# Performance work log

Measured on AMD Instinct MI355X. Metric: run time of the kernel, lower is better.

## Reference

```python
import jax, jax.numpy as jnp
import numpy as np

N, D, B, E, K, H, C = 100000, 256, 20000, 16, 3, 256, 40  # m = K = 3


def setup_inputs() -> dict:
    key = jax.random.key(0)
    ks = jax.random.split(key, 11)
    return {
        "nodes": jax.random.randint(ks[0], (B,), 0, N, dtype=jnp.int32),
        "structure": jax.random.randint(ks[1], (B, E, K), 0, N, dtype=jnp.int32),
        "X": jax.random.normal(ks[2], (N, D), dtype=jnp.float32),
        "beta": jax.random.uniform(ks[3], (1,), dtype=jnp.float32),
        "w_att_w": jax.random.normal(ks[4], (1,), dtype=jnp.float32),
        "w_att_b": jax.random.normal(ks[5], (1,), dtype=jnp.float32),
        "lin_W": jax.random.normal(ks[6], (H, D), dtype=jnp.float32) * 0.05,
        "lin_b": jax.random.normal(ks[7], (H,), dtype=jnp.float32) * 0.05,
        "skip_W": jax.random.normal(ks[8], (H, D), dtype=jnp.float32) * 0.05,
        "cls_W": jax.random.normal(ks[9], (C, H), dtype=jnp.float32) * 0.05,
        "cls_b": jax.random.normal(ks[10], (C,), dtype=jnp.float32) * 0.05,
    }


def reference(nodes, structure, X, beta, w_att_w, w_att_b, lin_W, lin_b, skip_W, cls_W, cls_b):
    # --- TMessagePassing (batched over nodes and hyperedges) ---
    feats = X[structure]                                  # [B, E, K, D] gather
    # variance over nodes in the hyperedge (unbiased=False), mean over feature dim
    edge_var = jnp.var(feats, axis=2).mean(axis=-1)       # [B, E]
    att = jax.nn.sigmoid(w_att_w[0] * edge_var + w_att_b[0])  # [B, E]
    # len(edge) == m (K == m=3): msg = prod(feats[:-1], dim=0)
    msg = jnp.prod(feats[:, :, : K - 1, :], axis=2)       # [B, E, D]
    neigh = jnp.einsum("be,bed->bd", att, msg)            # sum of att * msg over edges
    # --- Encoder (combine == 'sum') ---
    self_feat = X[nodes]                                  # [B, D]
    h = self_feat + neigh
    enc = jax.nn.relu(h @ lin_W.T + lin_b)                # [B, H]
    enc = (1.0 - beta[0]) * enc + beta[0] * (self_feat @ skip_W.T)
    # --- classifier + log_softmax ---
    logits = enc @ cls_W.T + cls_b                        # [B, C]
    return jax.nn.log_softmax(logits, axis=1)
```

## Files before the change

kernel.cpp:

```cpp
#include <hip/hip_runtime.h>
#include <hip/hip_bf16.h>
#include <math.h>

#define Dn 256
#define En 16
#define Kn 3
#define Hn 256
#define Cn 40
#define CnP 48

typedef __attribute__((ext_vector_type(8)))  short bf16x8;
typedef __attribute__((ext_vector_type(4)))  float f32x4;
typedef __attribute__((ext_vector_type(16))) float f32x16;

static __device__ __forceinline__ float bf2f(unsigned short u) {
    return __uint_as_float(((unsigned)u) << 16);
}
static __device__ __forceinline__ unsigned short f2bfbits(float v) {
    __hip_bfloat16 hb = __float2bfloat16(v);
    return *reinterpret_cast<unsigned short*>(&hb);
}
static __device__ __forceinline__ unsigned pack2bf(float a, float b) {
    return (unsigned)f2bfbits(a) | ((unsigned)f2bfbits(b) << 16);
}
static __device__ __forceinline__ unsigned swz(unsigned boff) {
    return boff ^ (((boff >> 9) & 7u) << 4);
}

__global__ __launch_bounds__(256) void conv_all(
    const float* __restrict__ X, const float* __restrict__ linW,
    const float* __restrict__ skipW, const float* __restrict__ clsW,
    uint4* __restrict__ Xb, uint4* __restrict__ linWb,
    uint4* __restrict__ skipWb, uint4* __restrict__ clsWb,
    int x8, int w8)
{
    int t = blockIdx.x * 256 + threadIdx.x;
    const int c8 = (CnP * Hn) / 8;
    if (t < x8) {
        const float4* iv = reinterpret_cast<const float4*>(X);
        const float4 a = iv[(size_t)t * 2 + 0];
        const float4 b = iv[(size_t)t * 2 + 1];
        Xb[t] = (uint4){pack2bf(a.x, a.y), pack2bf(a.z, a.w),
                        pack2bf(b.x, b.y), pack2bf(b.z, b.w)};
        return;
    }
    t -= x8;
    if (t < w8) {
        const float4* iv = reinterpret_cast<const float4*>(linW);
        const float4 a = iv[(size_t)t * 2 + 0];
        const float4 b = iv[(size_t)t * 2 + 1];
        linWb[t] = (uint4){pack2bf(a.x, a.y), pack2bf(a.z, a.w),
                           pack2bf(b.x, b.y), pack2bf(b.z, b.w)};
        return;
    }
    t -= w8;
    if (t < w8) {
        const float4* iv = reinterpret_cast<const float4*>(skipW);
        const float4 a = iv[(size_t)t * 2 + 0];
        const float4 b = iv[(size_t)t * 2 + 1];
        skipWb[t] = (uint4){pack2bf(a.x, a.y), pack2bf(a.z, a.w),
                            pack2bf(b.x, b.y), pack2bf(b.z, b.w)};
        return;
    }
    t -= w8;
    if (t < c8) {
        const int row = t >> 5;
        if (row < Cn) {
            const float4* iv = reinterpret_cast<const float4*>(clsW);
            const float4 a = iv[(size_t)t * 2 + 0];
            const float4 b = iv[(size_t)t * 2 + 1];
            clsWb[t] = (uint4){pack2bf(a.x, a.y), pack2bf(a.z, a.w),
                               pack2bf(b.x, b.y), pack2bf(b.z, b.w)};
        } else {
            clsWb[t] = (uint4){0u, 0u, 0u, 0u};
        }
    }
}

__global__ __launch_bounds__(256) void mp_kernel_bf(
    const int* __restrict__ nodes, const int* __restrict__ structure,
    const uint2* __restrict__ Xb,
    const float* __restrict__ waw_p, const float* __restrict__ wab_p,
    uint2* __restrict__ h_out, uint2* __restrict__ self_out, int B)
{
    const int wave = threadIdx.x >> 6;
    const int lane = threadIdx.x & 63;
    const int b = blockIdx.x * 4 + wave;
    if (b >= B) return;
    const int ub = __builtin_amdgcn_readfirstlane(b);

    const float waw = waw_p[0];
    const float wab = wab_p[0];

    float4 neigh = make_float4(0.f, 0.f, 0.f, 0.f);
    const int* st = structure + (size_t)ub * (En * Kn);

    #pragma unroll 1
    for (int g = 0; g < En / 4; ++g) {
        int idx[12];
        #pragma unroll
        for (int u = 0; u < 12; ++u) idx[u] = st[g * 12 + u];

        uint2 r0[4], r1[4], r2[4];
        #pragma unroll
        for (int u = 0; u < 4; ++u) {
            r0[u] = Xb[(size_t)idx[u * 3 + 0] * (Dn / 4) + lane];
            r1[u] = Xb[(size_t)idx[u * 3 + 1] * (Dn / 4) + lane];
            r2[u] = Xb[(size_t)idx[u * 3 + 2] * (Dn / 4) + lane];
        }

        float pv[4];
        float4 msg[4];
        #pragma unroll
        for (int u = 0; u < 4; ++u) {
            float4 f0, f1, f2;
            f0.x = bf2f((unsigned short)(r0[u].x & 0xffff));
            f0.y = bf2f((unsigned short)(r0[u].x >> 16));
            f0.z = bf2f((unsigned short)(r0[u].y & 0xffff));
            f0.w = bf2f((unsigned short)(r0[u].y >> 16));
            f1.x = bf2f((unsigned short)(r1[u].x & 0xffff));
            f1.y = bf2f((unsigned short)(r1[u].x >> 16));
            f1.z = bf2f((unsigned short)(r1[u].y & 0xffff));
            f1.w = bf2f((unsigned short)(r1[u].y >> 16));
            f2.x = bf2f((unsigned short)(r2[u].x & 0xffff));
            f2.y = bf2f((unsigned short)(r2[u].x >> 16));
            f2.z = bf2f((unsigned short)(r2[u].y & 0xffff));
            f2.w = bf2f((unsigned short)(r2[u].y >> 16));

            float s2 = 0.f, cr = 0.f, tt;
            s2 = fmaf(f0.x, f0.x, s2); s2 = fmaf(f1.x, f1.x, s2); s2 = fmaf(f2.x, f2.x, s2);
            tt = f1.x + f2.x; cr = fmaf(f0.x, tt, cr); cr = fmaf(f1.x, f2.x, cr);
            s2 = fmaf(f0.y, f0.y, s2); s2 = fmaf(f1.y, f1.y, s2); s2 = fmaf(f2.y, f2.y, s2);
            tt = f1.y + f2.y; cr = fmaf(f0.y, tt, cr); cr = fmaf(f1.y, f2.y, cr);
            s2 = fmaf(f0.z, f0.z, s2); s2 = fmaf(f1.z, f1.z, s2); s2 = fmaf(f2.z, f2.z, s2);
            tt = f1.z + f2.z; cr = fmaf(f0.z, tt, cr); cr = fmaf(f1.z, f2.z, cr);
            s2 = fmaf(f0.w, f0.w, s2); s2 = fmaf(f1.w, f1.w, s2); s2 = fmaf(f2.w, f2.w, s2);
            tt = f1.w + f2.w; cr = fmaf(f0.w, tt, cr); cr = fmaf(f1.w, f2.w, cr);

            pv[u] = s2 - cr;
            msg[u].x = f0.x * f1.x;
            msg[u].y = f0.y * f1.y;
            msg[u].z = f0.z * f1.z;
            msg[u].w = f0.w * f1.w;
        }

        #pragma unroll
        for (int off = 32; off; off >>= 1) {
            #pragma unroll
            for (int u = 0; u < 4; ++u) pv[u] += __shfl_xor(pv[u], off);
        }

        #pragma unroll
        for (int u = 0; u < 4; ++u) {
            const float var_mean = pv[u] * (2.f / (9.f * (float)Dn));
            const float att = 1.f / (1.f + expf(-(waw * var_mean + wab)));
            neigh.x += att * msg[u].x;
            neigh.y += att * msg[u].y;
            neigh.z += att * msg[u].z;
            neigh.w += att * msg[u].w;
        }
    }

    const uint2 sv = Xb[(size_t)nodes[ub] * (Dn / 4) + lane];
    self_out[(size_t)b * (Dn / 4) + lane] = sv;
    const float sx = bf2f((unsigned short)(sv.x & 0xffff));
    const float sy = bf2f((unsigned short)(sv.x >> 16));
    const float sz = bf2f((unsigned short)(sv.y & 0xffff));
    const float sw = bf2f((unsigned short)(sv.y >> 16));
    uint2 o;
    o.x = pack2bf(sx + neigh.x, sy + neigh.y);
    o.y = pack2bf(sz + neigh.z, sw + neigh.w);
    h_out[(size_t)b * (Dn / 4) + lane] = o;
}

__global__ __launch_bounds__(256, 2) void enc_cls_fused(
    const unsigned short* __restrict__ hB,
    const unsigned short* __restrict__ selfB,
    const unsigned short* __restrict__ linWb, const float* __restrict__ linb,
    const unsigned short* __restrict__ skipWb, const float* __restrict__ beta_p,
    const unsigned short* __restrict__ clsWb,
    const float* __restrict__ clsb,
    float* __restrict__ out, int M)
{
    __shared__ unsigned short elds[32 * 256];

    const int w  = threadIdx.x >> 6;
    const int l  = threadIdx.x & 63;
    const int lr = l & 31;
    const int kh = l >> 5;
    const int row0 = blockIdx.x * 32;

    const int arow = row0 + lr;
    const int arc  = arow < M ? arow : (M - 1);
    const int bc0 = w * 64 + lr;
    const int bc1 = w * 64 + 32 + lr;

    f32x16 acc1[2], acc2[2];
    acc1[0] = (f32x16)(0.f); acc1[1] = (f32x16)(0.f);
    acc2[0] = (f32x16)(0.f); acc2[1] = (f32x16)(0.f);

    #pragma unroll 4
    for (int k0 = 0; k0 < Dn; k0 += 16) {
        const int ko = k0 + kh * 8;
        const bf16x8 a1  = *reinterpret_cast<const bf16x8*>(hB    + (size_t)arc * Dn + ko);
        const bf16x8 a2  = *reinterpret_cast<const bf16x8*>(selfB + (size_t)arc * Dn + ko);
        const bf16x8 b10 = *reinterpret_cast<const bf16x8*>(linWb  + (size_t)bc0 * Dn + ko);
        const bf16x8 b11 = *reinterpret_cast<const bf16x8*>(linWb  + (size_t)bc1 * Dn + ko);
        const bf16x8 b20 = *reinterpret_cast<const bf16x8*>(skipWb + (size_t)bc0 * Dn + ko);
        const bf16x8 b21 = *reinterpret_cast<const bf16x8*>(skipWb + (size_t)bc1 * Dn + ko);
        acc1[0] = __builtin_amdgcn_mfma_f32_32x32x16_bf16(a1, b10, acc1[0], 0, 0, 0);
        acc1[1] = __builtin_amdgcn_mfma_f32_32x32x16_bf16(a1, b11, acc1[1], 0, 0, 0);
        acc2[0] = __builtin_amdgcn_mfma_f32_32x32x16_bf16(a2, b20, acc2[0], 0, 0, 0);
        acc2[1] = __builtin_amdgcn_mfma_f32_32x32x16_bf16(a2, b21, acc2[1], 0, 0, 0);
    }

    const float beta = beta_p[0];
    const float omb = 1.f - beta;
    #pragma unroll
    for (int n = 0; n < 2; ++n) {
        const int col = w * 64 + n * 32 + lr;
        const float bias = linb[col];
        #pragma unroll
        for (int r = 0; r < 16; ++r) {
            const int rowl = (r & 3) + 8 * (r >> 2) + 4 * kh;
            const float c1 = fmaxf(acc1[n][r] + bias, 0.f);
            const unsigned short v = f2bfbits(omb * c1 + beta * acc2[n][r]);
            const unsigned boff = swz((unsigned)(rowl * 512 + col * 2));
            *reinterpret_cast<unsigned short*>(
                reinterpret_cast<char*>(elds) + boff) = v;
        }
    }
    __syncthreads();

    if (w < 2) {
        const int lr16 = l & 15;
        const int kg = l >> 4;
        const int rowl0 = w * 16 + lr16;

        f32x4 cacc[3];
        cacc[0] = (f32x4){0.f,0.f,0.f,0.f};
        cacc[1] = (f32x4){0.f,0.f,0.f,0.f};
        cacc[2] = (f32x4){0.f,0.f,0.f,0.f};

        #pragma unroll
        for (int k0 = 0; k0 < Hn; k0 += 32) {
            const int ko = k0 + kg * 8;
            const unsigned boff = swz((unsigned)(rowl0 * 512 + ko * 2));
            const bf16x8 a = *reinterpret_cast<const bf16x8*>(
                reinterpret_cast<const char*>(elds) + boff);
            #pragma unroll
            for (int t = 0; t < 3; ++t) {
                const bf16x8 bb = *reinterpret_cast<const bf16x8*>(
                    clsWb + (size_t)(t * 16 + lr16) * Hn + ko);
                cacc[t] = __builtin_amdgcn_mfma_f32_16x16x32_bf16(a, bb, cacc[t], 0, 0, 0);
            }
        }

        float bias3[3];
        #pragma unroll
        for (int t = 0; t < 3; ++t) {
            const int cb = t * 16 + lr16;
            bias3[t] = (cb < Cn) ? clsb[cb] : -INFINITY;
        }

        #pragma unroll
        for (int r = 0; r < 4; ++r) {
            float lg0 = cacc[0][r] + bias3[0];
            float lg1 = cacc[1][r] + bias3[1];
            float lg2 = cacc[2][r] + bias3[2];
            float mx = fmaxf(fmaxf(lg0, lg1), lg2);
            #pragma unroll
            for (int off = 8; off; off >>= 1) mx = fmaxf(mx, __shfl_xor(mx, off));
            float se = expf(lg0 - mx) + expf(lg1 - mx) + expf(lg2 - mx);
            #pragma unroll
            for (int off = 8; off; off >>= 1) se += __shfl_xor(se, off);
            const float lse = logf(se);

            const int row = row0 + w * 16 + kg * 4 + r;
            if (row < M) {
                if (lr16 < 8) out[(size_t)row * Cn + 32 + lr16] = lg2 - mx - lse;
                out[(size_t)row * Cn + lr16]      = lg0 - mx - lse;
                out[(size_t)row * Cn + 16 + lr16] = lg1 - mx - lse;
            }
        }
    }
}

__global__ __launch_bounds__(256) void mp_kernel_f32(
    const int* __restrict__ nodes, const int* __restrict__ structure,
    const float* __restrict__ X, const float* __restrict__ waw_p,
    const float* __restrict__ wab_p, float* __restrict__ h_out, int B)
{
    const int wave = threadIdx.x >> 6;
    const int lane = threadIdx.x & 63;
    const int b = blockIdx.x * 4 + wave;
    if (b >= B) return;
    const int ub = __builtin_amdgcn_readfirstlane(b);

    const float waw = waw_p[0];
    const float wab = wab_p[0];
    const float4* __restrict__ Xv = reinterpret_cast<const float4*>(X);

    float4 neigh = make_float4(0.f, 0.f, 0.f, 0.f);
    const int* st = structure + (size_t)ub * (En * Kn);

    #pragma unroll 1
    for (int e = 0; e < En; ++e) {
        const int i0 = st[e * 3 + 0];
        const int i1 = st[e * 3 + 1];
        const int i2 = st[e * 3 + 2];
        const float4 f0 = Xv[(size_t)i0 * (Dn / 4) + lane];
        const float4 f1 = Xv[(size_t)i1 * (Dn / 4) + lane];
        const float4 f2 = Xv[(size_t)i2 * (Dn / 4) + lane];
        float pv = 0.f;
        {
            float a, bb, c, m;
            a = f0.x; bb = f1.x; c = f2.x;
            m = (a + bb + c) * (1.f / 3.f);
            pv += (a * a + bb * bb + c * c) * (1.f / 3.f) - m * m;
            a = f0.y; bb = f1.y; c = f2.y;
            m = (a + bb + c) * (1.f / 3.f);
            pv += (a * a + bb * bb + c * c) * (1.f / 3.f) - m * m;
            a = f0.z; bb = f1.z; c = f2.z;
            m = (a + bb + c) * (1.f / 3.f);
            pv += (a * a + bb * bb + c * c) * (1.f / 3.f) - m * m;
            a = f0.w; bb = f1.w; c = f2.w;
            m = (a + bb + c) * (1.f / 3.f);
            pv += (a * a + bb * bb + c * c) * (1.f / 3.f) - m * m;
        }
        #pragma unroll
        for (int off = 32; off; off >>= 1) pv += __shfl_xor(pv, off);
        const float var_mean = pv * (1.f / (float)Dn);
        const float att = 1.f / (1.f + expf(-(waw * var_mean + wab)));
        neigh.x += att * f0.x * f1.x;
        neigh.y += att * f0.y * f1.y;
        neigh.z += att * f0.z * f1.z;
        neigh.w += att * f0.w * f1.w;
    }

    const float4 s = Xv[(size_t)nodes[ub] * (Dn / 4) + lane];
    float4 h;
    h.x = s.x + neigh.x; h.y = s.y + neigh.y;
    h.z = s.z + neigh.z; h.w = s.w + neigh.w;
    reinterpret_cast<float4*>(h_out)[(size_t)b * (Dn / 4) + lane] = h;
}

#define BM 64
#define BN 64
#define BKs 16
#define LDT 68

__global__ __launch_bounds__(256) void enc_gemm_f32(
    const float* __restrict__ hA, const int* __restrict__ nodes,
    const float* __restrict__ X,
    const float* __restrict__ linW, const float* __restrict__ linb,
    const float* __restrict__ skipW, const float* __restrict__ beta_p,
    float* __restrict__ enc2, int M)
{
    __shared__ float Ats1[BKs][LDT];
    __shared__ float Ats2[BKs][LDT];
    __shared__ float Bts1[BKs][LDT];
    __shared__ float Bts2[BKs][LDT];

    const int tid = threadIdx.x;
    const int tx = tid & 15;
    const int ty = tid >> 4;
    const int row0 = blockIdx.x * BM;
    const int col0 = blockIdx.y * BN;

    const int lr = tid >> 2;
    const int lc = tid & 3;

    const int arow = row0 + lr;
    const bool arow_ok = arow < M;
    const int self_row = arow_ok ? nodes[arow] : 0;

    float acc1[4][4] = {{0.f}}, acc2[4][4] = {{0.f}};

    for (int k0 = 0; k0 < Dn; k0 += BKs) {
        float4 a1v = make_float4(0.f, 0.f, 0.f, 0.f);
        float4 a2v = make_float4(0.f, 0.f, 0.f, 0.f);
        if (arow_ok) {
            a1v = *reinterpret_cast<const float4*>(hA + (size_t)arow * Dn + k0 + lc * 4);
            a2v = *reinterpret_cast<const float4*>(X + (size_t)self_row * Dn + k0 + lc * 4);
        }
        const float4 b1v = *reinterpret_cast<const float4*>(linW + (size_t)(col0 + lr) * Dn + k0 + lc * 4);
        const float4 b2v = *reinterpret_cast<const float4*>(skipW + (size_t)(col0 + lr) * Dn + k0 + lc * 4);

        __syncthreads();
        Ats1[lc * 4 + 0][lr] = a1v.x; Ats1[lc * 4 + 1][lr] = a1v.y;
        Ats1[lc * 4 + 2][lr] = a1v.z; Ats1[lc * 4 + 3][lr] = a1v.w;
        Ats2[lc * 4 + 0][lr] = a2v.x; Ats2[lc * 4 + 1][lr] = a2v.y;
        Ats2[lc * 4 + 2][lr] = a2v.z; Ats2[lc * 4 + 3][lr] = a2v.w;
        Bts1[lc * 4 + 0][lr] = b1v.x; Bts1[lc * 4 + 1][lr] = b1v.y;
        Bts1[lc * 4 + 2][lr] = b1v.z; Bts1[lc * 4 + 3][lr] = b1v.w;
        Bts2[lc * 4 + 0][lr] = b2v.x; Bts2[lc * 4 + 1][lr] = b2v.y;
        Bts2[lc * 4 + 2][lr] = b2v.z; Bts2[lc * 4 + 3][lr] = b2v.w;
        __syncthreads();

        #pragma unroll
        for (int kk = 0; kk < BKs; ++kk) {
            const float4 a1 = *reinterpret_cast<const float4*>(&Ats1[kk][ty * 4]);
            const float4 a2 = *reinterpret_cast<const float4*>(&Ats2[kk][ty * 4]);
            const float4 b1 = *reinterpret_cast<const float4*>(&Bts1[kk][tx * 4]);
            const float4 b2 = *reinterpret_cast<const float4*>(&Bts2[kk][tx * 4]);
            const float a1a[4] = {a1.x, a1.y, a1.z, a1.w};
            const float a2a[4] = {a2.x, a2.y, a2.z, a2.w};
            const float b1a[4] = {b1.x, b1.y, b1.z, b1.w};
            const float b2a[4] = {b2.x, b2.y, b2.z, b2.w};
            #pragma unroll
            for (int i = 0; i < 4; ++i)
                #pragma unroll
                for (int j = 0; j < 4; ++j) {
                    acc1[i][j] = fmaf(a1a[i], b1a[j], acc1[i][j]);
                    acc2[i][j] = fmaf(a2a[i], b2a[j], acc2[i][j]);
                }
        }
    }

    const float beta = beta_p[0];
    const float omb = 1.f - beta;
    #pragma unroll
    for (int i = 0; i < 4; ++i) {
        const int r = row0 + ty * 4 + i;
        if (r >= M) continue;
        #pragma unroll
        for (int j = 0; j < 4; ++j) {
            const int c = col0 + tx * 4 + j;
            float c1 = acc1[i][j] + linb[c];
            c1 = fmaxf(c1, 0.f);
            enc2[(size_t)r * Hn + c] = omb * c1 + beta * acc2[i][j];
        }
    }
}

__global__ __launch_bounds__(256) void cls_kernel_f32(
    const float* __restrict__ enc2, const float* __restrict__ clsW,
    const float* __restrict__ clsb, float* __restrict__ out, int B)
{
    const int wave = threadIdx.x >> 6;
    const int lane = threadIdx.x & 63;
    const int b = blockIdx.x * 4 + wave;
    if (b >= B) return;

    const float4 e = reinterpret_cast<const float4*>(enc2 + (size_t)b * Hn)[lane];
    const float4* __restrict__ clsWv = reinterpret_cast<const float4*>(clsW);

    float mylogit = -INFINITY;
    #pragma unroll
    for (int c0 = 0; c0 < Cn; c0 += 8) {
        float p[8];
        #pragma unroll
        for (int u = 0; u < 8; ++u) {
            const float4 wv = clsWv[(size_t)(c0 + u) * (Hn / 4) + lane];
            p[u] = e.x * wv.x + e.y * wv.y + e.z * wv.z + e.w * wv.w;
        }
        #pragma unroll
        for (int off = 32; off; off >>= 1) {
            #pragma unroll
            for (int u = 0; u < 8; ++u) p[u] += __shfl_xor(p[u], off);
        }
        #pragma unroll
        for (int u = 0; u < 8; ++u)
            if (lane == c0 + u) mylogit = p[u];
    }
    if (lane < Cn) mylogit += clsb[lane];

    float mx = mylogit;
    #pragma unroll
    for (int off = 32; off; off >>= 1) mx = fmaxf(mx, __shfl_xor(mx, off));
    float ex = (lane < Cn) ? expf(mylogit - mx) : 0.f;
    float se = ex;
    #pragma unroll
    for (int off = 32; off; off >>= 1) se += __shfl_xor(se, off);
    const float lse = logf(se);

    if (lane < Cn) out[(size_t)b * Cn + lane] = mylogit - mx - lse;
}

extern "C" void kernel_launch(void* const* d_in, const int* in_sizes, int n_in,
                              void* d_out, int out_size, void* d_ws, size_t ws_size,
                              hipStream_t stream) {
    const int*   nodes     = (const int*)d_in[0];
    const int*   structure = (const int*)d_in[1];
    const float* X         = (const float*)d_in[2];
    const float* beta      = (const float*)d_in[3];
    const float* waw       = (const float*)d_in[4];
    const float* wab       = (const float*)d_in[5];
    const float* linW      = (const float*)d_in[6];
    const float* linb      = (const float*)d_in[7];
    const float* skipW     = (const float*)d_in[8];
    const float* clsW      = (const float*)d_in[9];
    const float* clsb      = (const float*)d_in[10];
    float* out = (float*)d_out;

    const int B = in_sizes[0];
    const int Ntot = in_sizes[2];

    unsigned short* h_bf   = (unsigned short*)d_ws;
    unsigned short* selfb  = h_bf + (size_t)B * Dn;
    unsigned short* Xb     = selfb + (size_t)B * Dn;
    unsigned short* linWb  = Xb + (size_t)Ntot;
    unsigned short* skipWb = linWb + (size_t)Hn * Dn;
    unsigned short* clsWb  = skipWb + (size_t)Hn * Dn;

    const size_t need = ((size_t)B * Dn * 2 + (size_t)Ntot +
                         (size_t)Hn * Dn * 2 + (size_t)CnP * Hn) * 2;

    if (ws_size >= need) {
        const int x8 = Ntot / 8;
        const int w8 = (Hn * Dn) / 8;
        const int c8 = (CnP * Hn) / 8;
        const int G = x8 + 2 * w8 + c8;
        conv_all<<<(G + 255) / 256, 256, 0, stream>>>(
            X, linW, skipW, clsW,
            (uint4*)Xb, (uint4*)linWb, (uint4*)skipWb, (uint4*)clsWb, x8, w8);

        mp_kernel_bf<<<(B + 3) / 4, 256, 0, stream>>>(
            nodes, structure, (const uint2*)Xb, waw, wab,
            (uint2*)h_bf, (uint2*)selfb, B);

        enc_cls_fused<<<(B + 31) / 32, 256, 0, stream>>>(
            h_bf, selfb, linWb, linb, skipWb, beta, clsWb, clsb, out, B);
    } else {
        float* enc2 = (float*)d_ws;
        float* hf   = enc2 + (size_t)B * Hn;
        mp_kernel_f32<<<(B + 3) / 4, 256, 0, stream>>>(nodes, structure, X, waw, wab, hf, B);
        dim3 g2((B + BM - 1) / BM, Hn / BN);
        enc_gemm_f32<<<g2, 256, 0, stream>>>(hf, nodes, X, linW, linb, skipW, beta, enc2, B);
        cls_kernel_f32<<<(B + 3) / 4, 256, 0, stream>>>(enc2, clsW, clsb, out, B);
    }
}
```

Measured before the change: 138.4 us.

## Fuse message-passing gather into encoder/classifier GEMM kernel via LDS staging

Merges the per-node hypergraph message-passing kernel with the encoder+classifier MFMA kernel. Each 256-thread block gathers 32 rows (8 per wave), stores h and self features as bf16 into swizzled shared memory, then runs the two GEMMs and the log-softmax from LDS. The intermediate h/self global writes and reads and one launch go away. In exchange each block now does a serial gather phase before its MFMA phase, which limits overlap, and it uses more LDS, which may lower occupancy.

```diff
diff --git a/kernel.cpp b/kernel.cpp
--- a/kernel.cpp
+++ b/kernel.cpp
@@ -23,8 +23,8 @@
 static __device__ __forceinline__ unsigned pack2bf(float a, float b) {
     return (unsigned)f2bfbits(a) | ((unsigned)f2bfbits(b) << 16);
 }
-static __device__ __forceinline__ unsigned swz(unsigned boff) {
-    return boff ^ (((boff >> 9) & 7u) << 4);
+static __device__ __forceinline__ unsigned swz5(unsigned boff) {
+    return boff ^ (((boff >> 9) & 31u) << 4);
 }
 
 __global__ __launch_bounds__(256) void conv_all(
@@ -77,133 +77,134 @@
     }
 }
 
-__global__ __launch_bounds__(256) void mp_kernel_bf(
+__global__ __launch_bounds__(256, 4) void mp_enc_cls(
     const int* __restrict__ nodes, const int* __restrict__ structure,
     const uint2* __restrict__ Xb,
     const float* __restrict__ waw_p, const float* __restrict__ wab_p,
-    uint2* __restrict__ h_out, uint2* __restrict__ self_out, int B)
+    const unsigned short* __restrict__ linWb, const float* __restrict__ linb,
+    const unsigned short* __restrict__ skipWb, const float* __restrict__ beta_p,
+    const unsigned short* __restrict__ clsWb, const float* __restrict__ clsb,
+    float* __restrict__ out, int B)
 {
-    const int wave = threadIdx.x >> 6;
+    __shared__ unsigned short hlds[32 * 256];
+    __shared__ unsigned short slds[32 * 256];
+
+    const int wid  = threadIdx.x >> 6;
     const int lane = threadIdx.x & 63;
-    const int b = blockIdx.x * 4 + wave;
-    if (b >= B) return;
-    const int ub = __builtin_amdgcn_readfirstlane(b);
+    const int row0 = blockIdx.x * 32;
 
     const float waw = waw_p[0];
     const float wab = wab_p[0];
 
-    float4 neigh = make_float4(0.f, 0.f, 0.f, 0.f);
-    const int* st = structure + (size_t)ub * (En * Kn);
-
     #pragma unroll 1
-    for (int g = 0; g < En / 4; ++g) {
-        int idx[12];
-        #pragma unroll
-        for (int u = 0; u < 12; ++u) idx[u] = st[g * 12 + u];
-
-        uint2 r0[4], r1[4], r2[4];
-        #pragma unroll
-        for (int u = 0; u < 4; ++u) {
-            r0[u] = Xb[(size_t)idx[u * 3 + 0] * (Dn / 4) + lane];
-            r1[u] = Xb[(size_t)idx[u * 3 + 1] * (Dn / 4) + lane];
-            r2[u] = Xb[(size_t)idx[u * 3 + 2] * (Dn / 4) + lane];
-        }
-
-        float pv[4];
-        float4 msg[4];
-        #pragma unroll
-        for (int u = 0; u < 4; ++u) {
-            float4 f0, f1, f2;
-            f0.x = bf2f((unsigned short)(r0[u].x & 0xffff));
-            f0.y = bf2f((unsigned short)(r0[u].x >> 16));
-            f0.z = bf2f((unsigned short)(r0[u].y & 0xffff));
-            f0.w = bf2f((unsigned short)(r0[u].y >> 16));
-            f1.x = bf2f((unsigned short)(r1[u].x & 0xffff));
-            f1.y = bf2f((unsigned short)(r1[u].x >> 16));
-            f1.z = bf2f((unsigned short)(r1[u].y & 0xffff));
-            f1.w = bf2f((unsigned short)(r1[u].y >> 16));
-            f2.x = bf2f((unsigned short)(r2[u].x & 0xffff));
-            f2.y = bf2f((unsigned short)(r2[u].x >> 16));
-            f2.z = bf2f((unsigned short)(r2[u].y & 0xffff));
-            f2.w = bf2f((unsigned short)(r2[u].y >> 16));
-
-            float s2 = 0.f, cr = 0.f, tt;
-            s2 = fmaf(f0.x, f0.x, s2); s2 = fmaf(f1.x, f1.x, s2); s2 = fmaf(f2.x, f2.x, s2);
-            tt = f1.x + f2.x; cr = fmaf(f0.x, tt, cr); cr = fmaf(f1.x, f2.x, cr);
-            s2 = fmaf(f0.y, f0.y, s2); s2 = fmaf(f1.y, f1.y, s2); s2 = fmaf(f2.y, f2.y, s2);
-            tt = f1.y + f2.y; cr = fmaf(f0.y, tt, cr); cr = fmaf(f1.y, f2.y, cr);
-            s2 = fmaf(f0.z, f0.z, s2); s2 = fmaf(f1.z, f1.z, s2); s2 = fmaf(f2.z, f2.z, s2);
-            tt = f1.z + f2.z; cr = fmaf(f0.z, tt, cr); cr = fmaf(f1.z, f2.z, cr);
-            s2 = fmaf(f0.w, f0.w, s2); s2 = fmaf(f1.w, f1.w, s2); s2 = fmaf(f2.w, f2.w, s2);
-            tt = f1.w + f2.w; cr = fmaf(f0.w, tt, cr); cr = fmaf(f1.w, f2.w, cr);
-
-            pv[u] = s2 - cr;
-            msg[u].x = f0.x * f1.x;
-            msg[u].y = f0.y * f1.y;
-            msg[u].z = f0.z * f1.z;
-            msg[u].w = f0.w * f1.w;
-        }
-
-        #pragma unroll
-        for (int off = 32; off; off >>= 1) {
-            #pragma unroll
-            for (int u = 0; u < 4; ++u) pv[u] += __shfl_xor(pv[u], off);
-        }
-
-        #pragma unroll
-        for (int u = 0; u < 4; ++u) {
-            const float var_mean = pv[u] * (2.f / (9.f * (float)Dn));
-            const float att = 1.f / (1.f + expf(-(waw * var_mean + wab)));
-            neigh.x += att * msg[u].x;
-            neigh.y += att * msg[u].y;
-            neigh.z += att * msg[u].z;
-            neigh.w += att * msg[u].w;
-        }
-    }
-
-    const uint2 sv = Xb[(size_t)nodes[ub] * (Dn / 4) + lane];
-    self_out[(size_t)b * (Dn / 4) + lane] = sv;
-    const float sx = bf2f((unsigned short)(sv.x & 0xffff));
-    const float sy = bf2f((unsigned short)(sv.x >> 16));
-    const float sz = bf2f((unsigned short)(sv.y & 0xffff));
-    const float sw = bf2f((unsigned short)(sv.y >> 16));
-    uint2 o;
-    o.x = pack2bf(sx + neigh.x, sy + neigh.y);
-    o.y = pack2bf(sz + neigh.z, sw + neigh.w);
-    h_out[(size_t)b * (Dn / 4) + lane] = o;
-}
-
-__global__ __launch_bounds__(256, 2) void enc_cls_fused(
-    const unsigned short* __restrict__ hB,
-    const unsigned short* __restrict__ selfB,
-    const unsigned short* __restrict__ linWb, const float* __restrict__ linb,
-    const unsigned short* __restrict__ skipWb, const float* __restrict__ beta_p,
-    const unsigned short* __restrict__ clsWb,
-    const float* __restrict__ clsb,
-    float* __restrict__ out, int M)
-{
-    __shared__ unsigned short elds[32 * 256];
-
-    const int w  = threadIdx.x >> 6;
-    const int l  = threadIdx.x & 63;
-    const int lr = l & 31;
-    const int kh = l >> 5;
-    const int row0 = blockIdx.x * 32;
-
-    const int arow = row0 + lr;
-    const int arc  = arow < M ? arow : (M - 1);
-    const int bc0 = w * 64 + lr;
-    const int bc1 = w * 64 + 32 + lr;
+    for (int j = 0; j < 8; ++j) {
+        const int rowl = wid * 8 + j;
+        const int b = row0 + rowl;
+        if (b < B) {
+            const int ub = __builtin_amdgcn_readfirstlane(b);
+            const int* st = structure + (size_t)ub * (En * Kn);
+
+            float4 neigh = make_float4(0.f, 0.f, 0.f, 0.f);
+
+            #pragma unroll 1
+            for (int g = 0; g < En / 4; ++g) {
+                int idx[12];
+                #pragma unroll
+                for (int u = 0; u < 12; ++u) idx[u] = st[g * 12 + u];
+
+                uint2 r0[4], r1[4], r2[4];
+                #pragma unroll
+                for (int u = 0; u < 4; ++u) {
+                    r0[u] = Xb[(size_t)idx[u * 3 + 0] * (Dn / 4) + lane];
+                    r1[u] = Xb[(size_t)idx[u * 3 + 1] * (Dn / 4) + lane];
+                    r2[u] = Xb[(size_t)idx[u * 3 + 2] * (Dn / 4) + lane];
+                }
+
+                float pv[4];
+                float4 msg[4];
+                #pragma unroll
+                for (int u = 0; u < 4; ++u) {
+                    float4 f0, f1, f2;
+                    f0.x = bf2f((unsigned short)(r0[u].x & 0xffff));
+                    f0.y = bf2f((unsigned short)(r0[u].x >> 16));
+                    f0.z = bf2f((unsigned short)(r0[u].y & 0xffff));
+                    f0.w = bf2f((unsigned short)(r0[u].y >> 16));
+                    f1.x = bf2f((unsigned short)(r1[u].x & 0xffff));
+                    f1.y = bf2f((unsigned short)(r1[u].x >> 16));
+                    f1.z = bf2f((unsigned short)(r1[u].y & 0xffff));
+                    f1.w = bf2f((unsigned short)(r1[u].y >> 16));
+                    f2.x = bf2f((unsigned short)(r2[u].x & 0xffff));
+                    f2.y = bf2f((unsigned short)(r2[u].x >> 16));
+                    f2.z = bf2f((unsigned short)(r2[u].y & 0xffff));
+                    f2.w = bf2f((unsigned short)(r2[u].y >> 16));
+
+                    float s2 = 0.f, cr = 0.f, tt;
+                    s2 = fmaf(f0.x, f0.x, s2); s2 = fmaf(f1.x, f1.x, s2); s2 = fmaf(f2.x, f2.x, s2);
+                    tt = f1.x + f2.x; cr = fmaf(f0.x, tt, cr); cr = fmaf(f1.x, f2.x, cr);
+                    s2 = fmaf(f0.y, f0.y, s2); s2 = fmaf(f1.y, f1.y, s2); s2 = fmaf(f2.y, f2.y, s2);
+                    tt = f1.y + f2.y; cr = fmaf(f0.y, tt, cr); cr = fmaf(f1.y, f2.y, cr);
+                    s2 = fmaf(f0.z, f0.z, s2); s2 = fmaf(f1.z, f1.z, s2); s2 = fmaf(f2.z, f2.z, s2);
+                    tt = f1.z + f2.z; cr = fmaf(f0.z, tt, cr); cr = fmaf(f1.z, f2.z, cr);
+                    s2 = fmaf(f0.w, f0.w, s2); s2 = fmaf(f1.w, f1.w, s2); s2 = fmaf(f2.w, f2.w, s2);
+                    tt = f1.w + f2.w; cr = fmaf(f0.w, tt, cr); cr = fmaf(f1.w, f2.w, cr);
+
+                    pv[u] = s2 - cr;
+                    msg[u].x = f0.x * f1.x;
+                    msg[u].y = f0.y * f1.y;
+                    msg[u].z = f0.z * f1.z;
+                    msg[u].w = f0.w * f1.w;
+                }
+
+                #pragma unroll
+                for (int off = 32; off; off >>= 1) {
+                    #pragma unroll
+                    for (int u = 0; u < 4; ++u) pv[u] += __shfl_xor(pv[u], off);
+                }
+
+                #pragma unroll
+                for (int u = 0; u < 4; ++u) {
+                    const float var_mean = pv[u] * (2.f / (9.f * (float)Dn));
+                    const float att = 1.f / (1.f + expf(-(waw * var_mean + wab)));
+                    neigh.x += att * msg[u].x;
+                    neigh.y += att * msg[u].y;
+                    neigh.z += att * msg[u].z;
+                    neigh.w += att * msg[u].w;
+                }
+            }
+
+            const uint2 sv = Xb[(size_t)nodes[ub] * (Dn / 4) + lane];
+            const float sx = bf2f((unsigned short)(sv.x & 0xffff));
+            const float sy = bf2f((unsigned short)(sv.x >> 16));
+            const float sz = bf2f((unsigned short)(sv.y & 0xffff));
+            const float sw = bf2f((unsigned short)(sv.y >> 16));
+            uint2 o;
+            o.x = pack2bf(sx + neigh.x, sy + neigh.y);
+            o.y = pack2bf(sz + neigh.z, sw + neigh.w);
+
+            const unsigned boff = swz5((unsigned)(rowl * 512 + lane * 8));
+            *reinterpret_cast<uint2*>(reinterpret_cast<char*>(slds) + boff) = sv;
+            *reinterpret_cast<uint2*>(reinterpret_cast<char*>(hlds) + boff) = o;
+        }
+    }
+    __syncthreads();
+
+    const int lr = lane & 31;
+    const int kh = lane >> 5;
+    const int bc0 = wid * 64 + lr;
+    const int bc1 = wid * 64 + 32 + lr;
 
     f32x16 acc1[2], acc2[2];
     acc1[0] = (f32x16)(0.f); acc1[1] = (f32x16)(0.f);
     acc2[0] = (f32x16)(0.f); acc2[1] = (f32x16)(0.f);
 
-    #pragma unroll 4
+    #pragma unroll 2
     for (int k0 = 0; k0 < Dn; k0 += 16) {
         const int ko = k0 + kh * 8;
-        const bf16x8 a1  = *reinterpret_cast<const bf16x8*>(hB    + (size_t)arc * Dn + ko);
-        const bf16x8 a2  = *reinterpret_cast<const bf16x8*>(selfB + (size_t)arc * Dn + ko);
+        const unsigned aoff = swz5((unsigned)(lr * 512 + ko * 2));
+        const bf16x8 a1 = *reinterpret_cast<const bf16x8*>(
+            reinterpret_cast<const char*>(hlds) + aoff);
+        const bf16x8 a2 = *reinterpret_cast<const bf16x8*>(
+            reinterpret_cast<const char*>(slds) + aoff);
         const bf16x8 b10 = *reinterpret_cast<const bf16x8*>(linWb  + (size_t)bc0 * Dn + ko);
         const bf16x8 b11 = *reinterpret_cast<const bf16x8*>(linWb  + (size_t)bc1 * Dn + ko);
         const bf16x8 b20 = *reinterpret_cast<const bf16x8*>(skipWb + (size_t)bc0 * Dn + ko);
@@ -213,29 +214,30 @@
         acc2[0] = __builtin_amdgcn_mfma_f32_32x32x16_bf16(a2, b20, acc2[0], 0, 0, 0);
         acc2[1] = __builtin_amdgcn_mfma_f32_32x32x16_bf16(a2, b21, acc2[1], 0, 0, 0);
     }
+    __syncthreads();
 
     const float beta = beta_p[0];
     const float omb = 1.f - beta;
     #pragma unroll
     for (int n = 0; n < 2; ++n) {
-        const int col = w * 64 + n * 32 + lr;
+        const int col = wid * 64 + n * 32 + lr;
         const float bias = linb[col];
         #pragma unroll
         for (int r = 0; r < 16; ++r) {
             const int rowl = (r & 3) + 8 * (r >> 2) + 4 * kh;
             const float c1 = fmaxf(acc1[n][r] + bias, 0.f);
             const unsigned short v = f2bfbits(omb * c1 + beta * acc2[n][r]);
-            const unsigned boff = swz((unsigned)(rowl * 512 + col * 2));
+            const unsigned boff = swz5((unsigned)(rowl * 512 + col * 2));
             *reinterpret_cast<unsigned short*>(
-                reinterpret_cast<char*>(elds) + boff) = v;
+                reinterpret_cast<char*>(hlds) + boff) = v;
         }
     }
     __syncthreads();
 
-    if (w < 2) {
-        const int lr16 = l & 15;
-        const int kg = l >> 4;
-        const int rowl0 = w * 16 + lr16;
+    if (wid < 2) {
+        const int lr16 = lane & 15;
+        const int kg = lane >> 4;
+        const int rowl0 = wid * 16 + lr16;
 
         f32x4 cacc[3];
         cacc[0] = (f32x4){0.f,0.f,0.f,0.f};
@@ -245,9 +247,9 @@
         #pragma unroll
         for (int k0 = 0; k0 < Hn; k0 += 32) {
             const int ko = k0 + kg * 8;
-            const unsigned boff = swz((unsigned)(rowl0 * 512 + ko * 2));
+            const unsigned boff = swz5((unsigned)(rowl0 * 512 + ko * 2));
             const bf16x8 a = *reinterpret_cast<const bf16x8*>(
-                reinterpret_cast<const char*>(elds) + boff);
+                reinterpret_cast<const char*>(hlds) + boff);
             #pragma unroll
             for (int t = 0; t < 3; ++t) {
                 const bf16x8 bb = *reinterpret_cast<const bf16x8*>(
@@ -276,8 +278,8 @@
             for (int off = 8; off; off >>= 1) se += __shfl_xor(se, off);
             const float lse = logf(se);
 
-            const int row = row0 + w * 16 + kg * 4 + r;
-            if (row < M) {
+            const int row = row0 + wid * 16 + kg * 4 + r;
+            if (row < B) {
                 if (lr16 < 8) out[(size_t)row * Cn + 32 + lr16] = lg2 - mx - lse;
                 out[(size_t)row * Cn + lr16]      = lg0 - mx - lse;
                 out[(size_t)row * Cn + 16 + lr16] = lg1 - mx - lse;
@@ -497,15 +499,12 @@
     const int B = in_sizes[0];
     const int Ntot = in_sizes[2];
 
-    unsigned short* h_bf   = (unsigned short*)d_ws;
-    unsigned short* selfb  = h_bf + (size_t)B * Dn;
-    unsigned short* Xb     = selfb + (size_t)B * Dn;
+    unsigned short* Xb     = (unsigned short*)d_ws;
     unsigned short* linWb  = Xb + (size_t)Ntot;
     unsigned short* skipWb = linWb + (size_t)Hn * Dn;
     unsigned short* clsWb  = skipWb + (size_t)Hn * Dn;
 
-    const size_t need = ((size_t)B * Dn * 2 + (size_t)Ntot +
-                         (size_t)Hn * Dn * 2 + (size_t)CnP * Hn) * 2;
+    const size_t need = ((size_t)Ntot + (size_t)Hn * Dn * 2 + (size_t)CnP * Hn) * 2;
 
     if (ws_size >= need) {
         const int x8 = Ntot / 8;
@@ -516,12 +515,9 @@
             X, linW, skipW, clsW,
             (uint4*)Xb, (uint4*)linWb, (uint4*)skipWb, (uint4*)clsWb, x8, w8);
 
-        mp_kernel_bf<<<(B + 3) / 4, 256, 0, stream>>>(
+        mp_enc_cls<<<(B + 31) / 32, 256, 0, stream>>>(
             nodes, structure, (const uint2*)Xb, waw, wab,
-            (uint2*)h_bf, (uint2*)selfb, B);
-
-        enc_cls_fused<<<(B + 31) / 32, 256, 0, stream>>>(
-            h_bf, selfb, linWb, linb, skipWb, beta, clsWb, clsb, out, B);
+            linWb, linb, skipWb, beta, clsWb, clsb, out, B);
     } else {
         float* enc2 = (float*)d_ws;
         float* hf   = enc2 + (size_t)B * Hn;
```

Result: faster. 124.2 us (-10.3%).

## Shrink encoder row tile to 16 using 16x16x32 MFMA for higher occupancy

Applied to the files above, without the earlier changes.

The fused encoder+classifier kernel now processes 16 rows per block instead of 32, switching from 32x32x16 to 16x16x32 bf16 MFMA with four 16-column tiles per wave. This halves the shared staging buffer and the accumulator registers, and raises the launch-bounds occupancy hint from 2 to 8 blocks. The cost is twice as many blocks, each re-reading the full lin/skip weight matrices, so global and L2 traffic for weights doubles. The classifier stage now runs on a single wave per block.

```diff
diff --git a/kernel.cpp b/kernel.cpp
--- a/kernel.cpp
+++ b/kernel.cpp
@@ -11,7 +11,6 @@
 
 typedef __attribute__((ext_vector_type(8)))  short bf16x8;
 typedef __attribute__((ext_vector_type(4)))  float f32x4;
-typedef __attribute__((ext_vector_type(16))) float f32x16;
 
 static __device__ __forceinline__ float bf2f(unsigned short u) {
     return __uint_as_float(((unsigned)u) << 16);
@@ -23,8 +22,8 @@
 static __device__ __forceinline__ unsigned pack2bf(float a, float b) {
     return (unsigned)f2bfbits(a) | ((unsigned)f2bfbits(b) << 16);
 }
-static __device__ __forceinline__ unsigned swz(unsigned boff) {
-    return boff ^ (((boff >> 9) & 7u) << 4);
+static __device__ __forceinline__ unsigned swz4(unsigned boff) {
+    return boff ^ (((boff >> 9) & 15u) << 4);
 }
 
 __global__ __launch_bounds__(256) void conv_all(
@@ -173,7 +172,7 @@
     h_out[(size_t)b * (Dn / 4) + lane] = o;
 }
 
-__global__ __launch_bounds__(256, 2) void enc_cls_fused(
+__global__ __launch_bounds__(256, 8) void enc_cls16(
     const unsigned short* __restrict__ hB,
     const unsigned short* __restrict__ selfB,
     const unsigned short* __restrict__ linWb, const float* __restrict__ linb,
@@ -182,61 +181,58 @@
     const float* __restrict__ clsb,
     float* __restrict__ out, int M)
 {
-    __shared__ unsigned short elds[32 * 256];
-
-    const int w  = threadIdx.x >> 6;
-    const int l  = threadIdx.x & 63;
-    const int lr = l & 31;
-    const int kh = l >> 5;
-    const int row0 = blockIdx.x * 32;
-
-    const int arow = row0 + lr;
+    __shared__ unsigned short elds[16 * 256];
+
+    const int w    = threadIdx.x >> 6;
+    const int l    = threadIdx.x & 63;
+    const int lr16 = l & 15;
+    const int kg   = l >> 4;
+    const int row0 = blockIdx.x * 16;
+
+    const int arow = row0 + lr16;
     const int arc  = arow < M ? arow : (M - 1);
-    const int bc0 = w * 64 + lr;
-    const int bc1 = w * 64 + 32 + lr;
-
-    f32x16 acc1[2], acc2[2];
-    acc1[0] = (f32x16)(0.f); acc1[1] = (f32x16)(0.f);
-    acc2[0] = (f32x16)(0.f); acc2[1] = (f32x16)(0.f);
-
-    #pragma unroll 4
-    for (int k0 = 0; k0 < Dn; k0 += 16) {
-        const int ko = k0 + kh * 8;
-        const bf16x8 a1  = *reinterpret_cast<const bf16x8*>(hB    + (size_t)arc * Dn + ko);
-        const bf16x8 a2  = *reinterpret_cast<const bf16x8*>(selfB + (size_t)arc * Dn + ko);
-        const bf16x8 b10 = *reinterpret_cast<const bf16x8*>(linWb  + (size_t)bc0 * Dn + ko);
-        const bf16x8 b11 = *reinterpret_cast<const bf16x8*>(linWb  + (size_t)bc1 * Dn + ko);
-        const bf16x8 b20 = *reinterpret_cast<const bf16x8*>(skipWb + (size_t)bc0 * Dn + ko);
-        const bf16x8 b21 = *reinterpret_cast<const bf16x8*>(skipWb + (size_t)bc1 * Dn + ko);
-        acc1[0] = __builtin_amdgcn_mfma_f32_32x32x16_bf16(a1, b10, acc1[0], 0, 0, 0);
-        acc1[1] = __builtin_amdgcn_mfma_f32_32x32x16_bf16(a1, b11, acc1[1], 0, 0, 0);
-        acc2[0] = __builtin_amdgcn_mfma_f32_32x32x16_bf16(a2, b20, acc2[0], 0, 0, 0);
-        acc2[1] = __builtin_amdgcn_mfma_f32_32x32x16_bf16(a2, b21, acc2[1], 0, 0, 0);
+
+    f32x4 acc1[4], acc2[4];
+    #pragma unroll
+    for (int n = 0; n < 4; ++n) {
+        acc1[n] = (f32x4){0.f, 0.f, 0.f, 0.f};
+        acc2[n] = (f32x4){0.f, 0.f, 0.f, 0.f};
+    }
+
+    #pragma unroll 2
+    for (int k0 = 0; k0 < Dn; k0 += 32) {
+        const int ko = k0 + kg * 8;
+        const bf16x8 a1 = *reinterpret_cast<const bf16x8*>(hB    + (size_t)arc * Dn + ko);
+        const bf16x8 a2 = *reinterpret_cast<const bf16x8*>(selfB + (size_t)arc * Dn + ko);
+        #pragma unroll
+        for (int n = 0; n < 4; ++n) {
+            const int col = w * 64 + n * 16 + lr16;
+            const bf16x8 b1 = *reinterpret_cast<const bf16x8*>(linWb  + (size_t)col * Dn + ko);
+            const bf16x8 b2 = *reinterpret_cast<const bf16x8*>(skipWb + (size_t)col * Dn + ko);
+            acc1[n] = __builtin_amdgcn_mfma_f32_16x16x32_bf16(a1, b1, acc1[n], 0, 0, 0);
+            acc2[n] = __builtin_amdgcn_mfma_f32_16x16x32_bf16(a2, b2, acc2[n], 0, 0, 0);
+        }
     }
 
     const float beta = beta_p[0];
     const float omb = 1.f - beta;
     #pragma unroll
-    for (int n = 0; n < 2; ++n) {
-        const int col = w * 64 + n * 32 + lr;
+    for (int n = 0; n < 4; ++n) {
+        const int col = w * 64 + n * 16 + lr16;
         const float bias = linb[col];
         #pragma unroll
-        for (int r = 0; r < 16; ++r) {
-            const int rowl = (r & 3) + 8 * (r >> 2) + 4 * kh;
+        for (int r = 0; r < 4; ++r) {
+            const int rowl = kg * 4 + r;
             const float c1 = fmaxf(acc1[n][r] + bias, 0.f);
             const unsigned short v = f2bfbits(omb * c1 + beta * acc2[n][r]);
-            const unsigned boff = swz((unsigned)(rowl * 512 + col * 2));
+            const unsigned boff = swz4((unsigned)(rowl * 512 + col * 2));
             *reinterpret_cast<unsigned short*>(
                 reinterpret_cast<char*>(elds) + boff) = v;
         }
     }
     __syncthreads();
 
-    if (w < 2) {
-        const int lr16 = l & 15;
-        const int kg = l >> 4;
-        const int rowl0 = w * 16 + lr16;
-
+    if (w == 0) {
         f32x4 cacc[3];
         cacc[0] = (f32x4){0.f,0.f,0.f,0.f};
         cacc[1] = (f32x4){0.f,0.f,0.f,0.f};
@@ -245,7 +241,7 @@
         #pragma unroll
         for (int k0 = 0; k0 < Hn; k0 += 32) {
             const int ko = k0 + kg * 8;
-            const unsigned boff = swz((unsigned)(rowl0 * 512 + ko * 2));
+            const unsigned boff = swz4((unsigned)(lr16 * 512 + ko * 2));
             const bf16x8 a = *reinterpret_cast<const bf16x8*>(
                 reinterpret_cast<const char*>(elds) + boff);
             #pragma unroll
@@ -276,7 +272,7 @@
             for (int off = 8; off; off >>= 1) se += __shfl_xor(se, off);
             const float lse = logf(se);
 
-            const int row = row0 + w * 16 + kg * 4 + r;
+            const int row = row0 + kg * 4 + r;
             if (row < M) {
                 if (lr16 < 8) out[(size_t)row * Cn + 32 + lr16] = lg2 - mx - lse;
                 out[(size_t)row * Cn + lr16]      = lg0 - mx - lse;
@@ -520,7 +516,7 @@
             nodes, structure, (const uint2*)Xb, waw, wab,
             (uint2*)h_bf, (uint2*)selfb, B);
 
-        enc_cls_fused<<<(B + 31) / 32, 256, 0, stream>>>(
+        enc_cls16<<<(B + 15) / 16, 256, 0, stream>>>(
             h_bf, selfb, linWb, linb, skipWb, beta, clsWb, clsb, out, B);
     } else {
         float* enc2 = (float*)d_ws;
```

New measurement: 167.9 us. 1.21x slower.
